# Performance work log

Measured on AMD Instinct MI355X. Metric: run time of the kernel, lower is better.

Reference implementation:

```python
import jax, jax.numpy as jnp
import numpy as np

S, B, H = 2048, 32, 1024

def setup_inputs() -> dict:
    key = jax.random.key(0)
    k1, k2, k3, k4, k5 = jax.random.split(key, 5)
    hidden = jax.random.normal(k1, (B, H), dtype=jnp.float32)
    encoder_outputs = jax.random.normal(k2, (S, B, 2 * H), dtype=jnp.float32)
    # nn.Linear(3H, H): weight [H, 3H] in torch; store transposed [3H, H] for x @ W
    W = jax.random.normal(k3, (3 * H, H), dtype=jnp.float32) * (1.0 / np.sqrt(3 * H))
    b = jax.random.normal(k4, (H,), dtype=jnp.float32) * 0.01
    v = jax.random.uniform(k5, (H,), dtype=jnp.float32)  # torch.rand
    return {"hidden": hidden, "encoder_outputs": encoder_outputs, "W": W, "b": b, "v": v}

def reference(hidden, encoder_outputs, W, b, v):
    # hidden: [B, H]; encoder_outputs: [S, B, 2H]
    # Avoid materializing the repeated/concatenated tensor by splitting the linear:
    # cat(h_rep, enc) @ W == h @ W[:H] (broadcast over S) + enc @ W[H:]
    Wh, We = W[:H], W[H:]                         # [H, H], [2H, H]
    h_proj = hidden @ Wh + b                      # [B, H]
    energy = jnp.tanh(jnp.einsum('sbe,eh->sbh', encoder_outputs, We) + h_proj[None])  # [S, B, H]
    scores = jnp.einsum('sbh,h->bs', energy, v)   # [B, S]
    return jax.nn.softmax(scores, axis=1)
```

## Files before the change

kernel.cpp:

```cpp
#include <hip/hip_runtime.h>
#include <hip/hip_fp16.h>


typedef _Float16 half8 __attribute__((ext_vector_type(8)));
typedef float floatx4 __attribute__((ext_vector_type(4)));
typedef float f32x4 __attribute__((ext_vector_type(4)));

constexpr int SEQ = 2048;
constexpr int BAT = 32;
constexpr int HID = 1024;
constexpr int KDIM = 2048;
constexpr int MTOT = SEQ * BAT;
constexpr int KT = 64;

constexpr int B_BUF = 65536;
constexpr int A_PITCH = 64 * 16 + 16;
constexpr int A_BUF = 4 * A_PITCH;

__device__ __forceinline__ void glds16(const void* g, void* l) {
    __builtin_amdgcn_global_load_lds((__attribute__((address_space(1))) void*)(g),
                                     (__attribute__((address_space(3))) void*)(l), 16, 0, 0);
}

__global__ __launch_bounds__(256) void pack_b_kernel(const float* __restrict__ W,
                                                     _Float16* __restrict__ pb) {
    int t = blockIdx.x * blockDim.x + threadIdx.x;
    int nt = t >> 15;
    int rem = t & 32767;
    int kt = rem >> 9;
    int c = rem & 511;
    int g = c >> 7;
    int n = c & 127;
    int h = nt * 128 + n;
    int e0 = kt * 32 + g * 8;
    const float* src = W + (size_t)(1024 + e0) * 1024 + h;
    union { _Float16 hh[8]; uint4 u; } tmp;
#pragma unroll
    for (int j = 0; j < 8; ++j) tmp.hh[j] = (_Float16)src[(size_t)j * 1024];
    *(uint4*)(pb + (size_t)t * 8) = tmp.u;
}

__global__ __launch_bounds__(256) void hproj_kernel(const float* __restrict__ hidden,
                                                    const float* __restrict__ W,
                                                    const float* __restrict__ bias,
                                                    float* __restrict__ hp) {
    int b = blockIdx.x;
    int h0 = blockIdx.y * 64;
    int hl = threadIdx.x & 63;
    int ks = threadIdx.x >> 6;
    const float* hr = hidden + b * HID + ks * 256;
    const float* wc = W + (size_t)(ks * 256) * HID + h0 + hl;
    float acc = 0.0f;
#pragma unroll 8
    for (int e = 0; e < 256; ++e) acc += hr[e] * wc[(size_t)e * HID];
    __shared__ float red[256];
    red[threadIdx.x] = acc;
    __syncthreads();
    if (threadIdx.x < 64)
        hp[b * HID + h0 + threadIdx.x] = red[threadIdx.x] + red[64 + threadIdx.x] +
                                         red[128 + threadIdx.x] + red[192 + threadIdx.x] +
                                         bias[h0 + threadIdx.x];
}

__global__ __launch_bounds__(512, 2) void attn_gemm_kernel(
    const float* __restrict__ enc, const _Float16* __restrict__ pb,
    const float* __restrict__ hp, const float* __restrict__ v,
    float* __restrict__ score) {
    __shared__ char sB0v[B_BUF];
    __shared__ char sB1v[B_BUF];
    __shared__ char sA0v[A_BUF];
    __shared__ char sA1v[A_BUF];

    const int tid = threadIdx.x;
    const int lane = tid & 63;
    const int wv = tid >> 6;
    const int mt = blockIdx.x;
    const size_t r0 = (size_t)mt * 64;
    const int fm = lane & 15;
    const int fg = lane >> 4;

    const char* bg = (const char*)pb + (size_t)wv * KT * 8192;
    const int bl_off = wv * 8192;

    const int arow = tid >> 3;
    const int ac4 = tid & 7;
    const f32x4* agp = (const f32x4*)(enc + (r0 + arow) * KDIM) + ac4;
    const int awoff = (ac4 >> 1) * A_PITCH + arow * 16 + (ac4 & 1) * 8;

    const int ardoff = fg * A_PITCH + fm * 16;
    const int brdoff = wv * 8192 + fg * 2048 + fm * 16;

    floatx4 acc[4][8];
#pragma unroll
    for (int i = 0; i < 4; ++i)
#pragma unroll
        for (int j = 0; j < 8; ++j) acc[i][j] = (floatx4)0.0f;

    {
        f32x4 f = __builtin_nontemporal_load(agp);
        __builtin_amdgcn_sched_barrier(0);
        const char* g = bg;
        char* l0 = sB0v + bl_off;
#pragma unroll
        for (int j = 0; j < 8; ++j)
            glds16(g + (j * 64 + lane) * 16, l0 + (j * 64 + lane) * 16);
        __builtin_amdgcn_sched_barrier(0);
        union { _Float16 hh[4]; uint2 u; } pk;
        pk.hh[0] = (_Float16)f.x; pk.hh[1] = (_Float16)f.y;
        pk.hh[2] = (_Float16)f.z; pk.hh[3] = (_Float16)f.w;
        *(uint2*)(sA0v + awoff) = pk.u;
        asm volatile("s_waitcnt lgkmcnt(0)" ::: "memory");
        __builtin_amdgcn_s_barrier();
        __builtin_amdgcn_sched_barrier(0);
    }

#define KSTEP(KT_I, AB, BB, AN, BN, HAVE_NEXT)                                    \
    {                                                                             \
        f32x4 f;                                                                  \
        if (HAVE_NEXT) {                                                          \
            f = __builtin_nontemporal_load(agp + ((KT_I) + 1) * 8);               \
            __builtin_amdgcn_sched_barrier(0);                                    \
            const char* g = bg + (size_t)((KT_I) + 1) * 8192;                     \
            char* l0 = (BN) + bl_off;                                             \
            _Pragma("unroll")                                                     \
            for (int j = 0; j < 8; ++j)                                           \
                glds16(g + (j * 64 + lane) * 16, l0 + (j * 64 + lane) * 16);      \
            __builtin_amdgcn_sched_barrier(0);                                    \
                \
                \
            asm volatile("s_waitcnt vmcnt(9)" ::: "memory");                      \
        } else {                                                                  \
            asm volatile("s_waitcnt vmcnt(0)" ::: "memory");                      \
        }                                                                         \
        half8 af[4];                                                              \
        _Pragma("unroll")                                                         \
        for (int i = 0; i < 4; ++i)                                               \
            af[i] = *(const half8*)((AB) + ardoff + i * 256);                     \
        _Pragma("unroll")                                                         \
        for (int j = 0; j < 8; ++j) {                                             \
            half8 bf = *(const half8*)((BB) + brdoff + j * 256);                  \
            _Pragma("unroll")                                                     \
            for (int i = 0; i < 4; ++i)                                           \
                acc[i][j] =                                                       \
                    __builtin_amdgcn_mfma_f32_16x16x32_f16(af[i], bf, acc[i][j],  \
                                                           0, 0, 0);              \
        }                                                                         \
        __builtin_amdgcn_sched_barrier(0);                                        \
        if (HAVE_NEXT) {                                                          \
            union { _Float16 hh[4]; uint2 u; } pk;      \
            pk.hh[0] = (_Float16)f.x; pk.hh[1] = (_Float16)f.y;                   \
            pk.hh[2] = (_Float16)f.z; pk.hh[3] = (_Float16)f.w;                   \
            *(uint2*)((AN) + awoff) = pk.u;                                       \
        }                                                                         \
        asm volatile("s_waitcnt lgkmcnt(0)" ::: "memory");                        \
        __builtin_amdgcn_s_barrier();                                             \
        __builtin_amdgcn_sched_barrier(0);                                        \
    }

#pragma clang loop unroll(disable)
    for (int kt2 = 0; kt2 < KT; kt2 += 2) {
        KSTEP(kt2, sA0v, sB0v, sA1v, sB1v, true);
        KSTEP(kt2 + 1, sA1v, sB1v, sA0v, sB0v, (kt2 + 2 < KT));
    }
#undef KSTEP

    float sums[4][4];
#pragma unroll
    for (int i = 0; i < 4; ++i)
#pragma unroll
        for (int r = 0; r < 4; ++r) sums[i][r] = 0.0f;

#pragma unroll
    for (int j = 0; j < 8; ++j) {
        int h = wv * 128 + j * 16 + fm;
        float vv = v[h];
#pragma unroll
        for (int i = 0; i < 4; ++i) {
#pragma unroll
            for (int r = 0; r < 4; ++r) {
                int row = i * 16 + fg * 4 + r;
                int b = row & 31;
                float x = acc[i][j][r] + hp[b * HID + h];
                float e2 = __expf(2.0f * x);
                float th = 1.0f - 2.0f / (e2 + 1.0f);
                sums[i][r] += th * vv;
            }
        }
    }
#pragma unroll
    for (int i = 0; i < 4; ++i)
#pragma unroll
        for (int r = 0; r < 4; ++r) {
            float s = sums[i][r];
            s += __shfl_xor(s, 1);
            s += __shfl_xor(s, 2);
            s += __shfl_xor(s, 4);
            s += __shfl_xor(s, 8);
            sums[i][r] = s;
        }
    __syncthreads();
    float* red = (float*)sB0v;
    if (fm == 0) {
#pragma unroll
        for (int i = 0; i < 4; ++i)
#pragma unroll
            for (int r = 0; r < 4; ++r)
                red[wv * 64 + i * 16 + fg * 4 + r] = sums[i][r];
    }
    __syncthreads();
    if (tid < 64) {
        float tot = 0.0f;
#pragma unroll
        for (int w = 0; w < 8; ++w) tot += red[w * 64 + tid];
        score[r0 + tid] = tot;
    }
}

__global__ __launch_bounds__(256) void softmax_kernel(const float* __restrict__ score,
                                                      float* __restrict__ out) {
    int b = blockIdx.x;
    int tid = threadIdx.x;
    __shared__ float redm[4];
    __shared__ float reds[4];
    float vals[8];
    float mx = -1e30f;
#pragma unroll
    for (int k = 0; k < 8; ++k) {
        int s = k * 256 + tid;
        float a = score[(size_t)s * 32 + b];
        vals[k] = a;
        mx = fmaxf(mx, a);
    }
    for (int d = 1; d < 64; d <<= 1) mx = fmaxf(mx, __shfl_xor(mx, d));
    int wv = tid >> 6;
    if ((tid & 63) == 0) redm[wv] = mx;
    __syncthreads();
    mx = fmaxf(fmaxf(redm[0], redm[1]), fmaxf(redm[2], redm[3]));
    float sum = 0.0f;
#pragma unroll
    for (int k = 0; k < 8; ++k) {
        vals[k] = __expf(vals[k] - mx);
        sum += vals[k];
    }
    for (int d = 1; d < 64; d <<= 1) sum += __shfl_xor(sum, d);
    if ((tid & 63) == 0) reds[wv] = sum;
    __syncthreads();
    sum = reds[0] + reds[1] + reds[2] + reds[3];
    float inv = 1.0f / sum;
#pragma unroll
    for (int k = 0; k < 8; ++k) out[b * SEQ + k * 256 + tid] = vals[k] * inv;
}

extern "C" void kernel_launch(void* const* d_in, const int* in_sizes, int n_in,
                              void* d_out, int out_size, void* d_ws, size_t ws_size,
                              hipStream_t stream) {
    const float* hidden = (const float*)d_in[0];
    const float* enc    = (const float*)d_in[1];
    const float* W      = (const float*)d_in[2];
    const float* bias   = (const float*)d_in[3];
    const float* v      = (const float*)d_in[4];
    float* out = (float*)d_out;

    char* ws = (char*)d_ws;
    _Float16* packB = (_Float16*)ws;
    float* hp       = (float*)(ws + (4u << 20));
    float* score    = (float*)(ws + (4u << 20) + (128u << 10));

    pack_b_kernel<<<1024, 256, 0, stream>>>(W, packB);
    hproj_kernel<<<dim3(32, 16), 256, 0, stream>>>(hidden, W, bias, hp);
    attn_gemm_kernel<<<MTOT / 64, 512, 0, stream>>>(enc, packB, hp, v, score);
    softmax_kernel<<<BAT, 256, 0, stream>>>(score, out);
}
```

Before: 1.017 ms.

## Retile attention GEMM to 128-row M tiles with N split across two blocks

Each block now covers 128 rows of the encoder and half of the hidden dimension (512 columns) instead of 64 rows and the full 1024 columns. The two N halves write partial scores that the softmax kernel adds together. Blocks are ordered so that groups of four M tiles share the same weight half, which should improve reuse of B in L2. This cuts the per-block B tile and LDS size, but each block now loads twice as many A rows per k-step, and every encoder row is read by two blocks instead of one.

```diff
diff --git a/kernel.cpp b/kernel.cpp
--- a/kernel.cpp
+++ b/kernel.cpp
@@ -13,8 +13,8 @@
 constexpr int MTOT = SEQ * BAT;
 constexpr int KT = 64;
 
-constexpr int B_BUF = 65536;
-constexpr int A_PITCH = 64 * 16 + 16;
+constexpr int B_BUF = 32768;
+constexpr int A_PITCH = 128 * 16 + 16;
 constexpr int A_BUF = 4 * A_PITCH;
 
 __device__ __forceinline__ void glds16(const void* g, void* l) {
@@ -25,13 +25,13 @@
 __global__ __launch_bounds__(256) void pack_b_kernel(const float* __restrict__ W,
                                                      _Float16* __restrict__ pb) {
     int t = blockIdx.x * blockDim.x + threadIdx.x;
-    int nt = t >> 15;
-    int rem = t & 32767;
-    int kt = rem >> 9;
-    int c = rem & 511;
-    int g = c >> 7;
-    int n = c & 127;
-    int h = nt * 128 + n;
+    int nt2 = t >> 14;
+    int rem = t & 16383;
+    int kt = rem >> 8;
+    int c = rem & 255;
+    int g = c >> 6;
+    int n = c & 63;
+    int h = nt2 * 64 + n;
     int e0 = kt * 32 + g * 8;
     const float* src = W + (size_t)(1024 + e0) * 1024 + h;
     union { _Float16 hh[8]; uint4 u; } tmp;
@@ -74,41 +74,53 @@
     const int tid = threadIdx.x;
     const int lane = tid & 63;
     const int wv = tid >> 6;
-    const int mt = blockIdx.x;
-    const size_t r0 = (size_t)mt * 64;
+    const int bx = blockIdx.x;
+    const int q = bx & 7;
+    const int ch = q >> 2;
+    const int mt = (bx >> 3) * 4 + (q & 3);
+    const size_t r0 = (size_t)mt * 128;
     const int fm = lane & 15;
     const int fg = lane >> 4;
-
-    const char* bg = (const char*)pb + (size_t)wv * KT * 8192;
-    const int bl_off = wv * 8192;
-
-    const int arow = tid >> 3;
+    const int nt2 = ch * 8 + wv;
+
+    const char* bg = (const char*)pb + (size_t)nt2 * KT * 4096;
+    const int bl_off = wv * 4096;
+
+    const int arow0 = tid >> 3;
+    const int arow1 = arow0 + 64;
     const int ac4 = tid & 7;
-    const f32x4* agp = (const f32x4*)(enc + (r0 + arow) * KDIM) + ac4;
-    const int awoff = (ac4 >> 1) * A_PITCH + arow * 16 + (ac4 & 1) * 8;
+    const f32x4* agp0 = (const f32x4*)(enc + (r0 + arow0) * KDIM) + ac4;
+    const f32x4* agp1 = (const f32x4*)(enc + (r0 + arow1) * KDIM) + ac4;
+    const int g4 = ac4 >> 1, sub = ac4 & 1;
+    const int awoff0 = g4 * A_PITCH + arow0 * 16 + sub * 8;
+    const int awoff1 = g4 * A_PITCH + arow1 * 16 + sub * 8;
 
     const int ardoff = fg * A_PITCH + fm * 16;
-    const int brdoff = wv * 8192 + fg * 2048 + fm * 16;
-
-    floatx4 acc[4][8];
-#pragma unroll
-    for (int i = 0; i < 4; ++i)
-#pragma unroll
-        for (int j = 0; j < 8; ++j) acc[i][j] = (floatx4)0.0f;
+    const int brdoff = wv * 4096 + fg * 1024 + fm * 16;
+
+    floatx4 acc[8][4];
+#pragma unroll
+    for (int i = 0; i < 8; ++i)
+#pragma unroll
+        for (int j = 0; j < 4; ++j) acc[i][j] = (floatx4)0.0f;
 
     {
-        f32x4 f = __builtin_nontemporal_load(agp);
+        f32x4 f0 = __builtin_nontemporal_load(agp0);
+        f32x4 f1 = __builtin_nontemporal_load(agp1);
         __builtin_amdgcn_sched_barrier(0);
         const char* g = bg;
         char* l0 = sB0v + bl_off;
 #pragma unroll
-        for (int j = 0; j < 8; ++j)
+        for (int j = 0; j < 4; ++j)
             glds16(g + (j * 64 + lane) * 16, l0 + (j * 64 + lane) * 16);
         __builtin_amdgcn_sched_barrier(0);
-        union { _Float16 hh[4]; uint2 u; } pk;
-        pk.hh[0] = (_Float16)f.x; pk.hh[1] = (_Float16)f.y;
-        pk.hh[2] = (_Float16)f.z; pk.hh[3] = (_Float16)f.w;
-        *(uint2*)(sA0v + awoff) = pk.u;
+        union { _Float16 hh[4]; uint2 u; } pk0, pk1;
+        pk0.hh[0] = (_Float16)f0.x; pk0.hh[1] = (_Float16)f0.y;
+        pk0.hh[2] = (_Float16)f0.z; pk0.hh[3] = (_Float16)f0.w;
+        *(uint2*)(sA0v + awoff0) = pk0.u;
+        pk1.hh[0] = (_Float16)f1.x; pk1.hh[1] = (_Float16)f1.y;
+        pk1.hh[2] = (_Float16)f1.z; pk1.hh[3] = (_Float16)f1.w;
+        *(uint2*)(sA0v + awoff1) = pk1.u;
         asm volatile("s_waitcnt lgkmcnt(0)" ::: "memory");
         __builtin_amdgcn_s_barrier();
         __builtin_amdgcn_sched_barrier(0);
@@ -116,41 +128,45 @@
 
 #define KSTEP(KT_I, AB, BB, AN, BN, HAVE_NEXT)                                    \
     {                                                                             \
-        f32x4 f;                                                                  \
+        f32x4 f0, f1;                                                             \
         if (HAVE_NEXT) {                                                          \
-            f = __builtin_nontemporal_load(agp + ((KT_I) + 1) * 8);               \
+            f0 = __builtin_nontemporal_load(agp0 + ((KT_I) + 1) * 8);             \
+            f1 = __builtin_nontemporal_load(agp1 + ((KT_I) + 1) * 8);             \
             __builtin_amdgcn_sched_barrier(0);                                    \
-            const char* g = bg + (size_t)((KT_I) + 1) * 8192;                     \
+            const char* g = bg + (size_t)((KT_I) + 1) * 4096;                     \
             char* l0 = (BN) + bl_off;                                             \
             _Pragma("unroll")                                                     \
-            for (int j = 0; j < 8; ++j)                                           \
+            for (int j = 0; j < 4; ++j)                                           \
                 glds16(g + (j * 64 + lane) * 16, l0 + (j * 64 + lane) * 16);      \
             __builtin_amdgcn_sched_barrier(0);                                    \
-                \
-                \
-            asm volatile("s_waitcnt vmcnt(9)" ::: "memory");                      \
+                 \
+                 \
+            asm volatile("s_waitcnt vmcnt(6)" ::: "memory");                      \
         } else {                                                                  \
             asm volatile("s_waitcnt vmcnt(0)" ::: "memory");                      \
         }                                                                         \
-        half8 af[4];                                                              \
+        half8 af[8];                                                              \
         _Pragma("unroll")                                                         \
-        for (int i = 0; i < 4; ++i)                                               \
+        for (int i = 0; i < 8; ++i)                                               \
             af[i] = *(const half8*)((AB) + ardoff + i * 256);                     \
         _Pragma("unroll")                                                         \
-        for (int j = 0; j < 8; ++j) {                                             \
+        for (int j = 0; j < 4; ++j) {                                             \
             half8 bf = *(const half8*)((BB) + brdoff + j * 256);                  \
             _Pragma("unroll")                                                     \
-            for (int i = 0; i < 4; ++i)                                           \
+            for (int i = 0; i < 8; ++i)                                           \
                 acc[i][j] =                                                       \
                     __builtin_amdgcn_mfma_f32_16x16x32_f16(af[i], bf, acc[i][j],  \
                                                            0, 0, 0);              \
         }                                                                         \
         __builtin_amdgcn_sched_barrier(0);                                        \
         if (HAVE_NEXT) {                                                          \
-            union { _Float16 hh[4]; uint2 u; } pk;      \
-            pk.hh[0] = (_Float16)f.x; pk.hh[1] = (_Float16)f.y;                   \
-            pk.hh[2] = (_Float16)f.z; pk.hh[3] = (_Float16)f.w;                   \
-            *(uint2*)((AN) + awoff) = pk.u;                                       \
+            union { _Float16 hh[4]; uint2 u; } pk0, pk1;                          \
+            pk0.hh[0] = (_Float16)f0.x; pk0.hh[1] = (_Float16)f0.y;               \
+            pk0.hh[2] = (_Float16)f0.z; pk0.hh[3] = (_Float16)f0.w;               \
+            *(uint2*)((AN) + awoff0) = pk0.u;                                     \
+            pk1.hh[0] = (_Float16)f1.x; pk1.hh[1] = (_Float16)f1.y;               \
+            pk1.hh[2] = (_Float16)f1.z; pk1.hh[3] = (_Float16)f1.w;               \
+            *(uint2*)((AN) + awoff1) = pk1.u;                                     \
         }                                                                         \
         asm volatile("s_waitcnt lgkmcnt(0)" ::: "memory");                        \
         __builtin_amdgcn_s_barrier();                                             \
@@ -164,18 +180,18 @@
     }
 #undef KSTEP
 
-    float sums[4][4];
-#pragma unroll
-    for (int i = 0; i < 4; ++i)
+    float sums[8][4];
+#pragma unroll
+    for (int i = 0; i < 8; ++i)
 #pragma unroll
         for (int r = 0; r < 4; ++r) sums[i][r] = 0.0f;
 
 #pragma unroll
-    for (int j = 0; j < 8; ++j) {
-        int h = wv * 128 + j * 16 + fm;
+    for (int j = 0; j < 4; ++j) {
+        int h = ch * 512 + wv * 64 + j * 16 + fm;
         float vv = v[h];
 #pragma unroll
-        for (int i = 0; i < 4; ++i) {
+        for (int i = 0; i < 8; ++i) {
 #pragma unroll
             for (int r = 0; r < 4; ++r) {
                 int row = i * 16 + fg * 4 + r;
@@ -188,7 +204,7 @@
         }
     }
 #pragma unroll
-    for (int i = 0; i < 4; ++i)
+    for (int i = 0; i < 8; ++i)
 #pragma unroll
         for (int r = 0; r < 4; ++r) {
             float s = sums[i][r];
@@ -202,17 +218,17 @@
     float* red = (float*)sB0v;
     if (fm == 0) {
 #pragma unroll
-        for (int i = 0; i < 4; ++i)
+        for (int i = 0; i < 8; ++i)
 #pragma unroll
             for (int r = 0; r < 4; ++r)
-                red[wv * 64 + i * 16 + fg * 4 + r] = sums[i][r];
-    }
-    __syncthreads();
-    if (tid < 64) {
+                red[wv * 128 + i * 16 + fg * 4 + r] = sums[i][r];
+    }
+    __syncthreads();
+    if (tid < 128) {
         float tot = 0.0f;
 #pragma unroll
-        for (int w = 0; w < 8; ++w) tot += red[w * 64 + tid];
-        score[r0 + tid] = tot;
+        for (int w = 0; w < 8; ++w) tot += red[w * 128 + tid];
+        score[(size_t)ch * MTOT + r0 + tid] = tot;
     }
 }
 
@@ -227,7 +243,7 @@
 #pragma unroll
     for (int k = 0; k < 8; ++k) {
         int s = k * 256 + tid;
-        float a = score[(size_t)s * 32 + b];
+        float a = score[(size_t)s * 32 + b] + score[(size_t)MTOT + (size_t)s * 32 + b];
         vals[k] = a;
         mx = fmaxf(mx, a);
     }
@@ -268,6 +284,6 @@
 
     pack_b_kernel<<<1024, 256, 0, stream>>>(W, packB);
     hproj_kernel<<<dim3(32, 16), 256, 0, stream>>>(hidden, W, bias, hp);
-    attn_gemm_kernel<<<MTOT / 64, 512, 0, stream>>>(enc, packB, hp, v, score);
+    attn_gemm_kernel<<<1024, 512, 0, stream>>>(enc, packB, hp, v, score);
     softmax_kernel<<<BAT, 256, 0, stream>>>(score, out);
 }
```

Result: faster. 991.5 us (-2.5%).
